# Kernel optimization log

Hardware: AMD Instinct MI355X
Metric: run time of the kernel (lower is better)

The kernel has to match this reference:

```python
import jax, jax.numpy as jnp
import numpy as np

SEQ_LEN = 128
EMBED_DIM = 1024
BATCH = 128


def setup_inputs() -> dict:
    key = jax.random.key(0)
    ks = jax.random.split(key, 9)
    d = EMBED_DIM
    s = 0.02
    return {
        "x": jax.random.normal(ks[0], (BATCH, SEQ_LEN * d), dtype=jnp.float32),
        "Wq": jax.random.normal(ks[1], (d, d), dtype=jnp.float32) * s,
        "bq": jax.random.normal(ks[2], (d,), dtype=jnp.float32) * s,
        "Wk": jax.random.normal(ks[3], (d, d), dtype=jnp.float32) * s,
        "bk": jax.random.normal(ks[4], (d,), dtype=jnp.float32) * s,
        "Wv": jax.random.normal(ks[5], (d, d), dtype=jnp.float32) * s,
        "bv": jax.random.normal(ks[6], (d,), dtype=jnp.float32) * s,
        "Wo": jax.random.normal(ks[7], (d, d), dtype=jnp.float32) * s,
        "bo": jax.random.normal(ks[8], (d,), dtype=jnp.float32) * s,
    }


def reference(x, Wq, bq, Wk, bk, Wv, bv, Wo, bo):
    b = x.shape[0]
    d = EMBED_DIM
    xs = x.reshape(b, SEQ_LEN, d)  # [B, S, D]
    # torch Linear: y = x @ W.T + b
    Q = jnp.einsum("bsd,ed->bse", xs, Wq) + bq
    K = jnp.einsum("bsd,ed->bse", xs, Wk) + bk
    V = jnp.einsum("bsd,ed->bse", xs, Wv) + bv
    scores = jnp.einsum("bse,bte->bst", Q, K) / jnp.sqrt(jnp.float32(d))
    weights = jax.nn.softmax(scores, axis=-1)
    attended = jnp.einsum("bst,bte->bse", weights, V)
    out = jnp.einsum("bse,fe->bsf", attended, Wo) + bo
    return out.reshape(b, -1)
```

## Files before the change

### kernel.cpp

```cpp
#include <hip/hip_runtime.h>
#include <hip/hip_bf16.h>

typedef __attribute__((ext_vector_type(8))) __bf16 bf16x8;
typedef __attribute__((ext_vector_type(4))) __bf16 bf16x4;
typedef __attribute__((ext_vector_type(4))) float f32x4;

#define SEQ 128
#define DIM 1024
#define BATCH 128
#define MTOT (BATCH * SEQ)

__device__ __forceinline__ void gload16(const void* g, void* l) {
    __builtin_amdgcn_global_load_lds(
        (const __attribute__((address_space(1))) void*)g,
        (__attribute__((address_space(3))) void*)l, 16, 0, 0);
}

#define BARRIER() do { asm volatile("" ::: "memory"); __builtin_amdgcn_s_barrier(); asm volatile("" ::: "memory"); } while (0)
#define WAITV(N) asm volatile("s_waitcnt vmcnt(" #N ")" ::: "memory")
#define MFMA(a, b, c) __builtin_amdgcn_mfma_f32_16x16x32_bf16(a, b, c, 0, 0, 0)

__global__ void cast_f32_bf16(const float* __restrict__ in, __bf16* __restrict__ out, int n) {
    int i = (blockIdx.x * blockDim.x + threadIdx.x) * 8;
    if (i >= n) return;
    float4 f0 = *reinterpret_cast<const float4*>(in + i);
    float4 f1 = *reinterpret_cast<const float4*>(in + i + 4);
    bf16x8 o;
    o[0] = (__bf16)f0.x; o[1] = (__bf16)f0.y; o[2] = (__bf16)f0.z; o[3] = (__bf16)f0.w;
    o[4] = (__bf16)f1.x; o[5] = (__bf16)f1.y; o[6] = (__bf16)f1.z; o[7] = (__bf16)f1.w;
    *reinterpret_cast<bf16x8*>(out + i) = o;
}

template <int MODE>
__global__ __launch_bounds__(512, 1) void gemm256(const __bf16* __restrict__ A,
                                                  const __bf16* __restrict__ W,
                                                  const float* __restrict__ bias,
                                                  void* __restrict__ Cout) {
    const int K = 1024, N = 1024;
    __shared__ __bf16 lds[3][4][4096];
    const int tid = threadIdx.x, wave = tid >> 6, lane = tid & 63;
    const int wr = wave >> 2, wc = wave & 3;
    const int lr = lane & 15;
    const int lkb = ((lane >> 4) & 3) * 16;
    const int bid = blockIdx.x;
    const int swz = (bid & 7) * 32 + (bid >> 3);
    const int m0 = (swz >> 2) * 256, n0 = (swz & 3) * 256;
    const int rloc = wave * 16 + (lane >> 2);
    const int cbs  = ((((lane & 3) << 4) ^ (((lane >> 3) & 3) << 4)) >> 1);
    const __bf16* pA = A + (size_t)(m0 + rloc) * K + cbs;
    const __bf16* pB = W + (size_t)(n0 + rloc) * K + cbs;
    const int wo = wave * 512;

    f32x4 acc[8][4] = {};

#define LDF(SLOT, R) (*reinterpret_cast<const bf16x8*>( \
        reinterpret_cast<const char*>(SLOT) + (R) * 64 + (lkb ^ ((((R) >> 1) & 3) << 4))))
#define STAGE_A(SB, TS) do { gload16(pA + (TS) * 32, &lds[SB][0][wo]); \
                             gload16(pA + (size_t)128 * 1024 + (TS) * 32, &lds[SB][1][wo]); } while (0)
#define STAGE_B(SB, TS) do { gload16(pB + (TS) * 32, &lds[SB][2][wo]); \
                             gload16(pB + (size_t)128 * 1024 + (TS) * 32, &lds[SB][3][wo]); } while (0)

#define TILE(RB, SB, TS, DOSTAGE, VMSTMT) do { \
    const __bf16* As_ = &lds[RB][wr][0]; \
    const __bf16* Bs_ = &lds[RB][2 + (wc >> 1)][0]; \
    const int bb_ = (wc & 1) * 64; \
    bf16x8 a0 = LDF(As_, 0 * 16 + lr), a1 = LDF(As_, 1 * 16 + lr); \
    bf16x8 a2 = LDF(As_, 2 * 16 + lr), a3 = LDF(As_, 3 * 16 + lr); \
    bf16x8 b0 = LDF(Bs_, bb_ + 0 * 16 + lr), b1 = LDF(Bs_, bb_ + 1 * 16 + lr); \
    bf16x8 b2 = LDF(Bs_, bb_ + 2 * 16 + lr), b3 = LDF(Bs_, bb_ + 3 * 16 + lr); \
    if (DOSTAGE) STAGE_A(SB, TS); \
    BARRIER(); \
    __builtin_amdgcn_s_setprio(1); \
    acc[0][0] = MFMA(a0, b0, acc[0][0]); acc[0][1] = MFMA(a0, b1, acc[0][1]); \
    acc[0][2] = MFMA(a0, b2, acc[0][2]); acc[0][3] = MFMA(a0, b3, acc[0][3]); \
    acc[1][0] = MFMA(a1, b0, acc[1][0]); acc[1][1] = MFMA(a1, b1, acc[1][1]); \
    acc[1][2] = MFMA(a1, b2, acc[1][2]); acc[1][3] = MFMA(a1, b3, acc[1][3]); \
    acc[2][0] = MFMA(a2, b0, acc[2][0]); acc[2][1] = MFMA(a2, b1, acc[2][1]); \
    acc[2][2] = MFMA(a2, b2, acc[2][2]); acc[2][3] = MFMA(a2, b3, acc[2][3]); \
    acc[3][0] = MFMA(a3, b0, acc[3][0]); acc[3][1] = MFMA(a3, b1, acc[3][1]); \
    acc[3][2] = MFMA(a3, b2, acc[3][2]); acc[3][3] = MFMA(a3, b3, acc[3][3]); \
    __builtin_amdgcn_s_setprio(0); \
    BARRIER(); \
    a0 = LDF(As_, 4 * 16 + lr); a1 = LDF(As_, 5 * 16 + lr); \
    a2 = LDF(As_, 6 * 16 + lr); a3 = LDF(As_, 7 * 16 + lr); \
    if (DOSTAGE) STAGE_B(SB, TS); \
    BARRIER(); \
    __builtin_amdgcn_s_setprio(1); \
    acc[4][0] = MFMA(a0, b0, acc[4][0]); acc[4][1] = MFMA(a0, b1, acc[4][1]); \
    acc[4][2] = MFMA(a0, b2, acc[4][2]); acc[4][3] = MFMA(a0, b3, acc[4][3]); \
    acc[5][0] = MFMA(a1, b0, acc[5][0]); acc[5][1] = MFMA(a1, b1, acc[5][1]); \
    acc[5][2] = MFMA(a1, b2, acc[5][2]); acc[5][3] = MFMA(a1, b3, acc[5][3]); \
    acc[6][0] = MFMA(a2, b0, acc[6][0]); acc[6][1] = MFMA(a2, b1, acc[6][1]); \
    acc[6][2] = MFMA(a2, b2, acc[6][2]); acc[6][3] = MFMA(a2, b3, acc[6][3]); \
    acc[7][0] = MFMA(a3, b0, acc[7][0]); acc[7][1] = MFMA(a3, b1, acc[7][1]); \
    acc[7][2] = MFMA(a3, b2, acc[7][2]); acc[7][3] = MFMA(a3, b3, acc[7][3]); \
    __builtin_amdgcn_s_setprio(0); \
    VMSTMT; \
    BARRIER(); \
} while (0)

    STAGE_A(0, 0); STAGE_B(0, 0);
    STAGE_A(1, 1); STAGE_B(1, 1);
    WAITV(4);
    BARRIER();

    for (int it = 0; it < 10; ++it) {
        const int t = it * 3;
        TILE(0, 2, t + 2, 1, WAITV(4));
        TILE(1, 0, t + 3, 1, WAITV(4));
        TILE(2, 1, t + 4, 1, WAITV(4));
    }
    TILE(0, 0, 0, 0, WAITV(0));
    TILE(1, 0, 0, 0, (void)0);

    const int rbase = (lane >> 4) * 4;
    #pragma unroll
    for (int ri = 0; ri < 8; ++ri) {
        #pragma unroll
        for (int j = 0; j < 4; ++j) {
            const int gc  = n0 + wc * 64 + j * 16 + lr;
            const float bv = bias[gc];
            const int grb = m0 + wr * 128 + ri * 16 + rbase;
            if (MODE == 0) {
                __bf16* C = (__bf16*)Cout;
                #pragma unroll
                for (int r = 0; r < 4; ++r)
                    C[(size_t)(grb + r) * N + gc] = (__bf16)(acc[ri][j][r] + bv);
            } else if (MODE == 1) {
                float* C = (float*)Cout;
                #pragma unroll
                for (int r = 0; r < 4; ++r)
                    C[(size_t)(grb + r) * N + gc] = acc[ri][j][r] + bv;
            } else {
                __bf16* C = (__bf16*)Cout;
                const int b = grb >> 7, s = grb & 127;
                bf16x4 v;
                #pragma unroll
                for (int r = 0; r < 4; ++r) v[r] = (__bf16)(acc[ri][j][r] + bv);
                *reinterpret_cast<bf16x4*>(&C[((size_t)b * DIM + gc) * SEQ + s]) = v;
            }
        }
    }
#undef TILE
#undef STAGE_A
#undef STAGE_B
#undef LDF
}

__global__ __launch_bounds__(256) void attn_kernel(const __bf16* __restrict__ Q,
                                                   const __bf16* __restrict__ Km,
                                                   const __bf16* __restrict__ Vt,
                                                   __bf16* __restrict__ Ab) {
    __shared__ __align__(16) char smem[40960];
    float  (*Ssh)[132] = (float(*)[132])(smem);
    __bf16 (*Psh)[136] = (__bf16(*)[136])(smem + 16896);

    const int bid = blockIdx.x;
    const int logical = (bid & 7) * 64 + (bid >> 3);
    const int b = logical >> 2, rt = logical & 3;
    const int tid = threadIdx.x, wave = tid >> 6, lane = tid & 63;
    const int lr = lane & 15, lk = (lane >> 4) * 8, rbase = (lane >> 4) * 4;
    const __bf16* Qb = Q  + ((size_t)b * SEQ + rt * 32) * DIM;
    const __bf16* Kb = Km + (size_t)b * SEQ * DIM;
    const __bf16* Vb = Vt + (size_t)b * DIM * SEQ;

    const int csrc = ((lane & 7) * 16) ^ (((lane >> 3) & 7) << 4);

    f32x4 acc[2][2] = {};
    {
        auto stage_kq = [&](int buf, int c) {
            char* Kd = smem + buf * 20480 + wave * 4096;
            char* Qd = smem + buf * 20480 + 16384 + wave * 1024;
            const char* Ks = (const char*)Kb + (size_t)(wave * 32 + (lane >> 3)) * 2048 + c * 128 + csrc;
            #pragma unroll
            for (int q = 0; q < 4; ++q)
                gload16(Ks + (size_t)q * 8 * 2048, Kd + q * 1024);
            const char* Qs = (const char*)Qb + (size_t)(wave * 8 + (lane >> 3)) * 2048 + c * 128 + csrc;
            gload16(Qs, Qd);
        };
        stage_kq(0, 0);
        WAITV(0);
        BARRIER();
        for (int c = 0; c < 16; ++c) {
            const int rb = c & 1;
            if (c < 15) stage_kq(rb ^ 1, c + 1);
            const char* Kl = smem + rb * 20480;
            const char* Ql = Kl + 16384;
            bf16x8 qf[2][2], kf[2][2];
            #pragma unroll
            for (int i = 0; i < 2; ++i)
                #pragma unroll
                for (int ks = 0; ks < 2; ++ks) {
                    const int r = i * 16 + lr;
                    qf[i][ks] = *reinterpret_cast<const bf16x8*>(
                        Ql + r * 128 + ((ks * 64 + (lane >> 4) * 16) ^ ((r & 7) << 4)));
                }
            #pragma unroll
            for (int j = 0; j < 2; ++j)
                #pragma unroll
                for (int ks = 0; ks < 2; ++ks) {
                    const int r = wave * 32 + j * 16 + lr;
                    kf[j][ks] = *reinterpret_cast<const bf16x8*>(
                        Kl + r * 128 + ((ks * 64 + (lane >> 4) * 16) ^ ((r & 7) << 4)));
                }
            __builtin_amdgcn_s_setprio(1);
            #pragma unroll
            for (int i = 0; i < 2; ++i)
                #pragma unroll
                for (int j = 0; j < 2; ++j)
                    #pragma unroll
                    for (int ks = 0; ks < 2; ++ks)
                        acc[i][j] = MFMA(qf[i][ks], kf[j][ks], acc[i][j]);
            __builtin_amdgcn_s_setprio(0);
            WAITV(0);
            BARRIER();
        }
    }
    const float scale = 0.03125f;
    #pragma unroll
    for (int i = 0; i < 2; ++i)
        #pragma unroll
        for (int j = 0; j < 2; ++j)
            #pragma unroll
            for (int r = 0; r < 4; ++r)
                Ssh[i * 16 + rbase + r][wave * 32 + j * 16 + lr] = acc[i][j][r] * scale;
    __syncthreads();

    {
        const int row = tid >> 3;
        const int c0  = (tid & 7) * 16;
        float4 v0 = *reinterpret_cast<const float4*>(&Ssh[row][c0]);
        float4 v1 = *reinterpret_cast<const float4*>(&Ssh[row][c0 + 4]);
        float4 v2 = *reinterpret_cast<const float4*>(&Ssh[row][c0 + 8]);
        float4 v3 = *reinterpret_cast<const float4*>(&Ssh[row][c0 + 12]);
        float e[16] = {v0.x, v0.y, v0.z, v0.w, v1.x, v1.y, v1.z, v1.w,
                       v2.x, v2.y, v2.z, v2.w, v3.x, v3.y, v3.z, v3.w};
        float mx = e[0];
        #pragma unroll
        for (int u = 1; u < 16; ++u) mx = fmaxf(mx, e[u]);
        mx = fmaxf(mx, __shfl_xor(mx, 1));
        mx = fmaxf(mx, __shfl_xor(mx, 2));
        mx = fmaxf(mx, __shfl_xor(mx, 4));
        float s = 0.f;
        #pragma unroll
        for (int u = 0; u < 16; ++u) { e[u] = __expf(e[u] - mx); s += e[u]; }
        s += __shfl_xor(s, 1);
        s += __shfl_xor(s, 2);
        s += __shfl_xor(s, 4);
        const float inv = 1.f / s;
        bf16x8 p0, p1;
        #pragma unroll
        for (int u = 0; u < 8; ++u) { p0[u] = (__bf16)(e[u] * inv); p1[u] = (__bf16)(e[u + 8] * inv); }
        *reinterpret_cast<bf16x8*>(&Psh[row][c0])     = p0;
        *reinterpret_cast<bf16x8*>(&Psh[row][c0 + 8]) = p1;
    }
    __syncthreads();

    bf16x8 pf[2][4];
    #pragma unroll
    for (int i = 0; i < 2; ++i)
        #pragma unroll
        for (int ks = 0; ks < 4; ++ks)
            pf[i][ks] = *reinterpret_cast<const bf16x8*>(&Psh[i * 16 + lr][ks * 32 + lk]);
    __syncthreads();

    __bf16* Ao = Ab + ((size_t)b * SEQ + rt * 32) * DIM;
    {
        auto stage_v = [&](int buf, int c) {
            char* Vd = smem + buf * 16384 + wave * 4096;
            #pragma unroll
            for (int q = 0; q < 4; ++q) {
                const int rowl = wave * 16 + q * 4 + (lane >> 4);
                const char* Vs = (const char*)Vb + (size_t)(c * 64 + rowl) * 256 +
                                 (((lane & 15) * 16) ^ ((rowl & 7) << 4));
                gload16(Vs, Vd + q * 1024);
            }
        };
        stage_v(0, 0);
        WAITV(0);
        BARRIER();
        for (int c = 0; c < 16; ++c) {
            const int rb = c & 1;
            if (c < 15) stage_v(rb ^ 1, c + 1);
            const char* Vl = smem + rb * 16384;
            f32x4 a2[2] = {};
            const int r = wave * 16 + lr;
            #pragma unroll
            for (int ks = 0; ks < 4; ++ks) {
                bf16x8 vf = *reinterpret_cast<const bf16x8*>(
                    Vl + r * 256 + ((ks * 64 + (lane >> 4) * 16) ^ ((r & 7) << 4)));
                a2[0] = MFMA(pf[0][ks], vf, a2[0]);
                a2[1] = MFMA(pf[1][ks], vf, a2[1]);
            }
            const int n0 = c * 64 + wave * 16;
            #pragma unroll
            for (int i = 0; i < 2; ++i)
                #pragma unroll
                for (int rr = 0; rr < 4; ++rr)
                    Ao[(size_t)(i * 16 + rbase + rr) * DIM + n0 + lr] = (__bf16)a2[i][rr];
            WAITV(8);
            BARRIER();
        }
    }
}

extern "C" void kernel_launch(void* const* d_in, const int* in_sizes, int n_in,
                              void* d_out, int out_size, void* d_ws, size_t ws_size,
                              hipStream_t stream) {
    const float* x  = (const float*)d_in[0];
    const float* Wq = (const float*)d_in[1];
    const float* bq = (const float*)d_in[2];
    const float* Wk = (const float*)d_in[3];
    const float* bk = (const float*)d_in[4];
    const float* Wv = (const float*)d_in[5];
    const float* bv = (const float*)d_in[6];
    const float* Wo = (const float*)d_in[7];
    const float* bo = (const float*)d_in[8];

    char* ws = (char*)d_ws;
    const size_t MB = 1024 * 1024;
    __bf16* Xb  = (__bf16*)(ws);
    __bf16* Wqb = (__bf16*)(ws + 32 * MB);
    __bf16* Wkb = (__bf16*)(ws + 34 * MB);
    __bf16* Wvb = (__bf16*)(ws + 36 * MB);
    __bf16* Wob = (__bf16*)(ws + 38 * MB);
    __bf16* Qb  = (__bf16*)(ws + 40 * MB);
    __bf16* Kb  = (__bf16*)(ws + 72 * MB);
    __bf16* Vt  = (__bf16*)(ws + 104 * MB);
    __bf16* Ab  = Xb;

    const int nX = MTOT * DIM;
    const int nW = DIM * DIM;
    cast_f32_bf16<<<nX / 8 / 256, 256, 0, stream>>>(x, Xb, nX);
    cast_f32_bf16<<<nW / 8 / 256, 256, 0, stream>>>(Wq, Wqb, nW);
    cast_f32_bf16<<<nW / 8 / 256, 256, 0, stream>>>(Wk, Wkb, nW);
    cast_f32_bf16<<<nW / 8 / 256, 256, 0, stream>>>(Wv, Wvb, nW);
    cast_f32_bf16<<<nW / 8 / 256, 256, 0, stream>>>(Wo, Wob, nW);

    gemm256<0><<<256, 512, 0, stream>>>(Xb, Wqb, bq, (void*)Qb);
    gemm256<0><<<256, 512, 0, stream>>>(Xb, Wkb, bk, (void*)Kb);
    gemm256<2><<<256, 512, 0, stream>>>(Xb, Wvb, bv, (void*)Vt);

    attn_kernel<<<512, 256, 0, stream>>>(Qb, Kb, Vt, Ab);

    gemm256<1><<<256, 512, 0, stream>>>(Ab, Wob, bo, d_out);
}
```

Measured before the change: 199.7 us.

## Fuse X cast into merged QKV GEMM and batch weight casts

Drops the standalone f32-to-bf16 cast of the large activation matrix. A new fused QKV GEMM instead streams fp32 X tiles into LDS and converts them to bf16 while loading fragments. The three separate projection launches become one 768-block kernel, and the four weight casts merge into one 2D-grid launch. This removes a full write and re-read of a bf16 X copy and several launches. In exchange the fused GEMM reads twice as many bytes of A per tile, uses more LDS, and does conversion work in its inner loop; each block still reads X from global memory.

Measured after the change: 220.6 us. 1.1x slower.

```diff
diff --git a/kernel.cpp b/kernel.cpp
--- a/kernel.cpp
+++ b/kernel.cpp
@@ -20,15 +20,148 @@
 #define WAITV(N) asm volatile("s_waitcnt vmcnt(" #N ")" ::: "memory")
 #define MFMA(a, b, c) __builtin_amdgcn_mfma_f32_16x16x32_bf16(a, b, c, 0, 0, 0)
 
-__global__ void cast_f32_bf16(const float* __restrict__ in, __bf16* __restrict__ out, int n) {
+__global__ void cast_w4(const float* __restrict__ a, const float* __restrict__ b,
+                        const float* __restrict__ c, const float* __restrict__ d,
+                        __bf16* __restrict__ oa, __bf16* __restrict__ ob,
+                        __bf16* __restrict__ oc, __bf16* __restrict__ od, int n) {
+    const float* src; __bf16* dst;
+    switch (blockIdx.y) {
+        case 0: src = a; dst = oa; break;
+        case 1: src = b; dst = ob; break;
+        case 2: src = c; dst = oc; break;
+        default: src = d; dst = od; break;
+    }
     int i = (blockIdx.x * blockDim.x + threadIdx.x) * 8;
     if (i >= n) return;
-    float4 f0 = *reinterpret_cast<const float4*>(in + i);
-    float4 f1 = *reinterpret_cast<const float4*>(in + i + 4);
+    float4 f0 = *reinterpret_cast<const float4*>(src + i);
+    float4 f1 = *reinterpret_cast<const float4*>(src + i + 4);
     bf16x8 o;
     o[0] = (__bf16)f0.x; o[1] = (__bf16)f0.y; o[2] = (__bf16)f0.z; o[3] = (__bf16)f0.w;
     o[4] = (__bf16)f1.x; o[5] = (__bf16)f1.y; o[6] = (__bf16)f1.z; o[7] = (__bf16)f1.w;
-    *reinterpret_cast<bf16x8*>(out + i) = o;
+    *reinterpret_cast<bf16x8*>(dst + i) = o;
+}
+
+__device__ __forceinline__ bf16x8 ldfa(const char* bufA, int R, int ks32) {
+    const int sw = (R & 7) << 4;
+    f32x4 lo = *reinterpret_cast<const f32x4*>(bufA + ((R * 128 + ks32) ^ sw));
+    f32x4 hi = *reinterpret_cast<const f32x4*>(bufA + ((R * 128 + ks32 + 16) ^ sw));
+    bf16x8 o;
+    o[0] = (__bf16)lo[0]; o[1] = (__bf16)lo[1]; o[2] = (__bf16)lo[2]; o[3] = (__bf16)lo[3];
+    o[4] = (__bf16)hi[0]; o[5] = (__bf16)hi[1]; o[6] = (__bf16)hi[2]; o[7] = (__bf16)hi[3];
+    return o;
+}
+
+__global__ __launch_bounds__(512, 1) void gemm_qkv(const float* __restrict__ X,
+        const __bf16* __restrict__ Wqb, const __bf16* __restrict__ Wkb, const __bf16* __restrict__ Wvb,
+        const float* __restrict__ bq, const float* __restrict__ bk, const float* __restrict__ bv,
+        __bf16* __restrict__ Qo, __bf16* __restrict__ Ko, __bf16* __restrict__ Vt) {
+    __shared__ char lds[3][49152];
+    const int tid = threadIdx.x, wave = tid >> 6, lane = tid & 63;
+    const int wr = wave >> 2, wc = wave & 3;
+    const int lr = lane & 15;
+    const int lkb  = ((lane >> 4) & 3) * 16;
+    const int ks32 = ((lane >> 4) & 3) * 32;
+    const unsigned bid = blockIdx.x;
+    const unsigned swz = (bid & 7) * 96 + (bid >> 3);
+    const int mt = swz / 12, nt = swz % 12;
+    const int m0 = mt * 256;
+    const int n0row = (nt & 3) * 256;
+    const int mid = nt >> 2;
+    const __bf16* Wsel = (mid == 0) ? Wqb : (mid == 1) ? Wkb : Wvb;
+    const float*  bsel = (mid == 0) ? bq  : (mid == 1) ? bk  : bv;
+
+    const int csrcA = ((lane & 7) * 16) ^ (((lane >> 3) & 7) << 4);
+    const int cbsB  = ((lane & 3) * 16) ^ (((lane >> 3) & 3) << 4);
+    const char* pAg = (const char*)X + (size_t)(m0 + wave * 32 + (lane >> 3)) * 4096 + csrcA;
+    const char* pBg = (const char*)Wsel + (size_t)(n0row + wave * 32 + (lane >> 2)) * 2048 + cbsB;
+
+    f32x4 acc[8][4] = {};
+
+#define QLDFB(R) (*reinterpret_cast<const bf16x8*>(bufB + (R) * 64 + (lkb ^ ((((R) >> 1) & 3) << 4))))
+#define QSTAGE_A(SB, TS) do { char* d_ = &lds[SB][0] + wave * 4096; const char* s_ = pAg + (size_t)(TS) * 128; \
+    gload16(s_, d_); gload16(s_ + 8 * 4096, d_ + 1024); \
+    gload16(s_ + 16 * 4096, d_ + 2048); gload16(s_ + 24 * 4096, d_ + 3072); } while (0)
+#define QSTAGE_B(SB, TS) do { char* d_ = &lds[SB][32768] + wave * 2048; const char* s_ = pBg + (size_t)(TS) * 64; \
+    gload16(s_, d_); gload16(s_ + 16 * 2048, d_ + 1024); } while (0)
+
+#define QTILE(RB, SB, TS, DOSTAGE, VMSTMT) do { \
+    const char* bufA = &lds[RB][0]; \
+    const char* bufB = &lds[RB][32768]; \
+    bf16x8 a0 = ldfa(bufA, wr * 128 + 0 * 16 + lr, ks32), a1 = ldfa(bufA, wr * 128 + 1 * 16 + lr, ks32); \
+    bf16x8 a2 = ldfa(bufA, wr * 128 + 2 * 16 + lr, ks32), a3 = ldfa(bufA, wr * 128 + 3 * 16 + lr, ks32); \
+    bf16x8 b0 = QLDFB(wc * 64 + 0 * 16 + lr), b1 = QLDFB(wc * 64 + 1 * 16 + lr); \
+    bf16x8 b2 = QLDFB(wc * 64 + 2 * 16 + lr), b3 = QLDFB(wc * 64 + 3 * 16 + lr); \
+    if (DOSTAGE) QSTAGE_A(SB, TS); \
+    BARRIER(); \
+    __builtin_amdgcn_s_setprio(1); \
+    acc[0][0] = MFMA(a0, b0, acc[0][0]); acc[0][1] = MFMA(a0, b1, acc[0][1]); \
+    acc[0][2] = MFMA(a0, b2, acc[0][2]); acc[0][3] = MFMA(a0, b3, acc[0][3]); \
+    acc[1][0] = MFMA(a1, b0, acc[1][0]); acc[1][1] = MFMA(a1, b1, acc[1][1]); \
+    acc[1][2] = MFMA(a1, b2, acc[1][2]); acc[1][3] = MFMA(a1, b3, acc[1][3]); \
+    acc[2][0] = MFMA(a2, b0, acc[2][0]); acc[2][1] = MFMA(a2, b1, acc[2][1]); \
+    acc[2][2] = MFMA(a2, b2, acc[2][2]); acc[2][3] = MFMA(a2, b3, acc[2][3]); \
+    acc[3][0] = MFMA(a3, b0, acc[3][0]); acc[3][1] = MFMA(a3, b1, acc[3][1]); \
+    acc[3][2] = MFMA(a3, b2, acc[3][2]); acc[3][3] = MFMA(a3, b3, acc[3][3]); \
+    __builtin_amdgcn_s_setprio(0); \
+    BARRIER(); \
+    a0 = ldfa(bufA, wr * 128 + 64 + 0 * 16 + lr, ks32); a1 = ldfa(bufA, wr * 128 + 64 + 1 * 16 + lr, ks32); \
+    a2 = ldfa(bufA, wr * 128 + 64 + 2 * 16 + lr, ks32); a3 = ldfa(bufA, wr * 128 + 64 + 3 * 16 + lr, ks32); \
+    if (DOSTAGE) QSTAGE_B(SB, TS); \
+    BARRIER(); \
+    __builtin_amdgcn_s_setprio(1); \
+    acc[4][0] = MFMA(a0, b0, acc[4][0]); acc[4][1] = MFMA(a0, b1, acc[4][1]); \
+    acc[4][2] = MFMA(a0, b2, acc[4][2]); acc[4][3] = MFMA(a0, b3, acc[4][3]); \
+    acc[5][0] = MFMA(a1, b0, acc[5][0]); acc[5][1] = MFMA(a1, b1, acc[5][1]); \
+    acc[5][2] = MFMA(a1, b2, acc[5][2]); acc[5][3] = MFMA(a1, b3, acc[5][3]); \
+    acc[6][0] = MFMA(a2, b0, acc[6][0]); acc[6][1] = MFMA(a2, b1, acc[6][1]); \
+    acc[6][2] = MFMA(a2, b2, acc[6][2]); acc[6][3] = MFMA(a2, b3, acc[6][3]); \
+    acc[7][0] = MFMA(a3, b0, acc[7][0]); acc[7][1] = MFMA(a3, b1, acc[7][1]); \
+    acc[7][2] = MFMA(a3, b2, acc[7][2]); acc[7][3] = MFMA(a3, b3, acc[7][3]); \
+    __builtin_amdgcn_s_setprio(0); \
+    VMSTMT; \
+    BARRIER(); \
+} while (0)
+
+    QSTAGE_A(0, 0); QSTAGE_B(0, 0);
+    QSTAGE_A(1, 1); QSTAGE_B(1, 1);
+    WAITV(6);
+    BARRIER();
+
+    for (int it = 0; it < 10; ++it) {
+        const int t = it * 3;
+        QTILE(0, 2, t + 2, 1, WAITV(6));
+        QTILE(1, 0, t + 3, 1, WAITV(6));
+        QTILE(2, 1, t + 4, 1, WAITV(6));
+    }
+    QTILE(0, 0, 0, 0, WAITV(0));
+    QTILE(1, 0, 0, 0, (void)0);
+
+    const int rbase = (lane >> 4) * 4;
+    #pragma unroll
+    for (int ri = 0; ri < 8; ++ri) {
+        #pragma unroll
+        for (int j = 0; j < 4; ++j) {
+            const int gcl = n0row + wc * 64 + j * 16 + lr;
+            const float bvv = bsel[gcl];
+            const int grb = m0 + wr * 128 + ri * 16 + rbase;
+            if (mid < 2) {
+                __bf16* C = (mid == 0) ? Qo : Ko;
+                #pragma unroll
+                for (int r = 0; r < 4; ++r)
+                    C[(size_t)(grb + r) * DIM + gcl] = (__bf16)(acc[ri][j][r] + bvv);
+            } else {
+                const int b = grb >> 7, s = grb & 127;
+                bf16x4 v;
+                #pragma unroll
+                for (int r = 0; r < 4; ++r) v[r] = (__bf16)(acc[ri][j][r] + bvv);
+                *reinterpret_cast<bf16x4*>(&Vt[((size_t)b * DIM + gcl) * SEQ + s]) = v;
+            }
+        }
+    }
+#undef QTILE
+#undef QSTAGE_A
+#undef QSTAGE_B
+#undef QLDFB
 }
 
 template <int MODE>
@@ -319,7 +452,7 @@
 
     char* ws = (char*)d_ws;
     const size_t MB = 1024 * 1024;
-    __bf16* Xb  = (__bf16*)(ws);
+    __bf16* Ab  = (__bf16*)(ws);
     __bf16* Wqb = (__bf16*)(ws + 32 * MB);
     __bf16* Wkb = (__bf16*)(ws + 34 * MB);
     __bf16* Wvb = (__bf16*)(ws + 36 * MB);
@@ -327,19 +460,11 @@
     __bf16* Qb  = (__bf16*)(ws + 40 * MB);
     __bf16* Kb  = (__bf16*)(ws + 72 * MB);
     __bf16* Vt  = (__bf16*)(ws + 104 * MB);
-    __bf16* Ab  = Xb;
-
-    const int nX = MTOT * DIM;
+
     const int nW = DIM * DIM;
-    cast_f32_bf16<<<nX / 8 / 256, 256, 0, stream>>>(x, Xb, nX);
-    cast_f32_bf16<<<nW / 8 / 256, 256, 0, stream>>>(Wq, Wqb, nW);
-    cast_f32_bf16<<<nW / 8 / 256, 256, 0, stream>>>(Wk, Wkb, nW);
-    cast_f32_bf16<<<nW / 8 / 256, 256, 0, stream>>>(Wv, Wvb, nW);
-    cast_f32_bf16<<<nW / 8 / 256, 256, 0, stream>>>(Wo, Wob, nW);
-
-    gemm256<0><<<256, 512, 0, stream>>>(Xb, Wqb, bq, (void*)Qb);
-    gemm256<0><<<256, 512, 0, stream>>>(Xb, Wkb, bk, (void*)Kb);
-    gemm256<2><<<256, 512, 0, stream>>>(Xb, Wvb, bv, (void*)Vt);
+    cast_w4<<<dim3(nW / 8 / 256, 4), 256, 0, stream>>>(Wq, Wk, Wv, Wo, Wqb, Wkb, Wvb, Wob, nW);
+
+    gemm_qkv<<<768, 512, 0, stream>>>(x, Wqb, Wkb, Wvb, bq, bk, bv, Qb, Kb, Vt);
 
     attn_kernel<<<512, 256, 0, stream>>>(Qb, Kb, Vt, Ab);
 
```
